# Kernel optimization log

Measured on AMD Instinct MI355X. Metric: run time of the kernel, lower is better.

The kernel has to match this reference:

```python
import jax, jax.numpy as jnp
import numpy as np

DIM = 1024
HEADS = 16
HEAD_DIM = DIM // HEADS
RANK = 16
ALPHA = 8.0
SCALING = ALPHA / RANK  # 0.5
SCALE = HEAD_DIM ** (-0.5)
B_, L_ = 2, 2048


def _proj_params(key, std=0.02):
    kW, kb, kA, kB = jax.random.split(key, 4)
    W = jax.random.normal(kW, (DIM, DIM), jnp.float32) * std   # [out, in]
    b = jax.random.normal(kb, (DIM,), jnp.float32) * std
    A = jax.random.normal(kA, (DIM, RANK), jnp.float32) * std  # [out, r]
    Bm = jax.random.normal(kB, (RANK, DIM), jnp.float32) * std # [r, in]
    return W, b, A, Bm


def setup_inputs() -> dict:
    key = jax.random.key(0)
    ks = jax.random.split(key, 6)
    x = jax.random.normal(ks[0], (B_, L_, DIM), jnp.float32)
    attn_bias = jax.random.normal(ks[1], (1, HEADS, L_, L_), jnp.float32) * 0.1
    inp = {"x": x, "attn_bias": attn_bias}
    for name, k in zip("qkvo", ks[2:6]):
        W, b, A, Bm = _proj_params(k)
        inp[f"W{name}"] = W
        inp[f"b{name}"] = b
        inp[f"A{name}"] = A
        inp[f"B{name}"] = Bm
    return inp


def _lora_linear(x, W, b, A, Bm):
    # y = x W^T + b + scaling * ((x @ A) @ B)   (matches torch LoRALinear)
    return x @ W.T + b + SCALING * ((x @ A) @ Bm)


def _split(x):
    B, L, D = x.shape
    return jnp.swapaxes(x.reshape(B, L, HEADS, HEAD_DIM), 1, 2)  # [B,H,L,hd]


def reference(x, attn_bias, Wq, bq, Aq, Bq, Wk, bk, Ak, Bk, Wv, bv, Av, Bv, Wo, bo, Ao, Bo):
    B, L, D = x.shape
    q = _split(_lora_linear(x, Wq, bq, Aq, Bq))
    k = _split(_lora_linear(x, Wk, bk, Ak, Bk))
    v = _split(_lora_linear(x, Wv, bv, Av, Bv))
    scores = jnp.einsum('bhld,bhmd->bhlm', q, k) * SCALE + attn_bias
    attn = jax.nn.softmax(scores, axis=-1)  # dropout p=0 -> identity
    out = jnp.einsum('bhlm,bhmd->bhld', attn, v)
    out = jnp.swapaxes(out, 1, 2).reshape(B, L, D)  # merge heads
    return _lora_linear(out, Wo, bo, Ao, Bo)
```

## Files before the change

### kernel.cpp

```cpp
#include <hip/hip_runtime.h>
#include <cstdint>

typedef __bf16 bf16;
typedef __bf16 bf16x8 __attribute__((ext_vector_type(8)));
typedef __bf16 bf16x4 __attribute__((ext_vector_type(4)));
typedef float  f32x4  __attribute__((ext_vector_type(4)));
typedef float  f32x16 __attribute__((ext_vector_type(16)));
typedef int    i32x4  __attribute__((ext_vector_type(4)));

#define DIM   1024
#define LSEQ  2048
#define NH    16
#define HD    64
#define NTOK  4096

#define AS1C(p) ((const __attribute__((address_space(1))) void*)(unsigned long long)(uintptr_t)(p))
#define AS3P(p) ((__attribute__((address_space(3))) void*)(unsigned int)(uintptr_t)(p))
#define SB0 __builtin_amdgcn_sched_barrier(0)

__device__ __forceinline__ f32x4 mfma16(bf16x8 a, bf16x8 b, f32x4 c) {
  return __builtin_amdgcn_mfma_f32_16x16x32_bf16(a, b, c, 0, 0, 0);
}
__device__ __forceinline__ f32x16 mfma32(bf16x8 a, bf16x8 b, f32x16 c) {
  return __builtin_amdgcn_mfma_f32_32x32x16_bf16(a, b, c, 0, 0, 0);
}
__device__ __forceinline__ int pk2(float a, float b) {
  unsigned short ua = __builtin_bit_cast(unsigned short, (bf16)a);
  unsigned short ub = __builtin_bit_cast(unsigned short, (bf16)b);
  return (int)ua | ((int)ub << 16);
}

__global__ __launch_bounds__(256) void k_cvt(const float* __restrict__ x,
                                             bf16* __restrict__ xb) {
  const int i = (blockIdx.x * 256 + threadIdx.x) * 4;
  const f32x4 v = *(const f32x4*)(x + i);
  bf16x4 o;
  o[0] = (bf16)v[0]; o[1] = (bf16)v[1]; o[2] = (bf16)v[2]; o[3] = (bf16)v[3];
  *(bf16x4*)(xb + i) = o;
}

struct WeffArgs {
  const float* W[4]; const float* A[4]; const float* B[4]; bf16* out[4];
};

__global__ __launch_bounds__(256) void k_weff(WeffArgs args) {
  const int o = blockIdx.x;
  const int z = blockIdx.y;
  const float* __restrict__ W  = args.W[z];
  const float* __restrict__ A  = args.A[z];
  const float* __restrict__ Bm = args.B[z];
  bf16* __restrict__ out = args.out[z];
  float Bo[16];
#pragma unroll
  for (int r = 0; r < 16; ++r) Bo[r] = Bm[r * DIM + o];
#pragma unroll
  for (int j = 0; j < 4; ++j) {
    const int d = j * 256 + (int)threadIdx.x;
    const float* Ar = A + (size_t)d * 16;
    float acc = 0.f;
#pragma unroll
    for (int r = 0; r < 16; ++r) acc += Ar[r] * Bo[r];
    out[(size_t)o * DIM + d] = (bf16)(W[(size_t)o * DIM + d] + 0.5f * acc);
  }
}

template <int NF, bool F32OUT>
__device__ __forceinline__ void gemm_body(const bf16* __restrict__ X,
                                          const bf16* __restrict__ W,
                                          const float* __restrict__ bias,
                                          void* __restrict__ out,
                                          float scale, int m0, int n0) {
  constexpr int BN = NF * 32;
  __shared__ __align__(16) bf16 As[128 * 32];
  __shared__ __align__(16) bf16 Bs[BN * 32];
  const int tid  = threadIdx.x;
  const int lane = tid & 63, w = tid >> 6;
  const int l15 = lane & 15, l4 = lane >> 4;
  const int wr = w >> 1, wc = w & 1;
  const int srow = w * 16 + (lane >> 2);
  const int scol = (lane & 3) * 8;

  f32x4 acc[4][NF] = {};
  const bf16* ag = X + (size_t)m0 * DIM;
  const bf16* bg = W + (size_t)n0 * DIM;

  for (int kt = 0; kt < DIM / 32; ++kt) {
    const int k0 = kt * 32;
#pragma unroll
    for (int j = 0; j < 2; ++j) {
      const int row = j * 64 + srow;
      __builtin_amdgcn_global_load_lds(AS1C(ag + (size_t)row * DIM + k0 + scol),
                                       AS3P(As + (j * 64 + w * 16) * 32), 16, 0, 0);
      if (j * 64 < BN)
        __builtin_amdgcn_global_load_lds(AS1C(bg + (size_t)row * DIM + k0 + scol),
                                         AS3P(Bs + (j * 64 + w * 16) * 32), 16, 0, 0);
    }
    __syncthreads();
    bf16x8 af[4], bfr[NF];
#pragma unroll
    for (int m = 0; m < 4; ++m)
      af[m] = *(const bf16x8*)(As + (wr * 64 + m * 16 + l15) * 32 + l4 * 8);
#pragma unroll
    for (int n = 0; n < NF; ++n)
      bfr[n] = *(const bf16x8*)(Bs + (wc * NF * 16 + n * 16 + l15) * 32 + l4 * 8);
#pragma unroll
    for (int m = 0; m < 4; ++m)
#pragma unroll
      for (int n = 0; n < NF; ++n)
        acc[m][n] = mfma16(af[m], bfr[n], acc[m][n]);
    __syncthreads();
  }

#pragma unroll
  for (int m = 0; m < 4; ++m) {
    const int r0 = m0 + wr * 64 + m * 16 + l4 * 4;
#pragma unroll
    for (int n = 0; n < NF; ++n) {
      const int c = n0 + wc * NF * 16 + n * 16 + l15;
      const float bc = bias[c];
#pragma unroll
      for (int t = 0; t < 4; ++t) {
        const float y = (acc[m][n][t] + bc) * scale;
        if constexpr (F32OUT)
          ((float*)out)[(size_t)(r0 + t) * DIM + c] = y;
        else
          ((bf16*)out)[(size_t)(r0 + t) * DIM + c] = (bf16)y;
      }
    }
  }
}

__global__ __launch_bounds__(256) void k_gemm_qkv(
    const bf16* __restrict__ xb, const bf16* __restrict__ weff,
    const float* __restrict__ bq, const float* __restrict__ bk,
    const float* __restrict__ bv,
    bf16* __restrict__ q, bf16* __restrict__ k, bf16* __restrict__ v) {
  const int z = blockIdx.z;
  const bf16* W = weff + (size_t)z * DIM * DIM;
  const float* bias = (z == 0) ? bq : (z == 1) ? bk : bv;
  bf16* out = (z == 0) ? q : (z == 1) ? k : v;
  const float scale = (z == 0) ? 0.125f : 1.0f;
  gemm_body<4, false>(xb, W, bias, out, scale, blockIdx.x * 128, blockIdx.y * 128);
}

__global__ __launch_bounds__(256) void k_gemm_o(
    const bf16* __restrict__ ctx, const bf16* __restrict__ weffo,
    const float* __restrict__ bo, float* __restrict__ out) {
  gemm_body<2, true>(ctx, weffo, bo, out, 1.0f, blockIdx.x * 128, blockIdx.y * 64);
}

__global__ __launch_bounds__(256) void k_vfrag(const bf16* __restrict__ v,
                                               const bf16* __restrict__ k,
                                               bf16* __restrict__ vf,
                                               bf16* __restrict__ kf) {
  const int lt = blockIdx.x, bh = blockIdx.y;
  const int b = bh >> 4, h = bh & 15;
  __shared__ __align__(16) bf16 tile[64][72];
  const int tid = threadIdx.x;
  const int r = tid >> 2, c0 = (tid & 3) * 16;
  const bf16* src = v + (size_t)(b * LSEQ + lt * 64) * DIM + h * HD;
  *(bf16x8*)(&tile[r][c0])     = *(const bf16x8*)(src + (size_t)r * DIM + c0);
  *(bf16x8*)(&tile[r][c0 + 8]) = *(const bf16x8*)(src + (size_t)r * DIM + c0 + 8);
  __syncthreads();
  const int w = tid >> 6, lane = tid & 63, l31 = lane & 31, hi = lane >> 5;
  {
    const int tt = w >> 1, n = w & 1;
    const int t = lt * 2 + tt;
#pragma unroll
    for (int c = 0; c < 2; ++c) {
      bf16 tmp[8];
#pragma unroll
      for (int j = 0; j < 8; ++j)
        tmp[j] = tile[tt * 32 + c * 16 + hi * 8 + j][n * 32 + l31];
      *(bf16x8*)(vf + ((((size_t)bh * 64 + t) * 4 + n * 2 + c) * 64 + lane) * 8) =
          *(bf16x8*)tmp;
    }
  }
  {
    const int t = lt * 2 + (w & 1);
    const bf16* krow = k + (size_t)(b * LSEQ + t * 32 + l31) * DIM + h * HD + hi * 8;
#pragma unroll
    for (int cc = 0; cc < 2; ++cc) {
      const int c = (w >> 1) + cc * 2;
      *(bf16x8*)(kf + ((((size_t)bh * 64 + t) * 4 + c) * 64 + lane) * 8) =
          *(const bf16x8*)(krow + c * 16);
    }
  }
}

__global__ __launch_bounds__(512, 1) void k_attn(
    const bf16* __restrict__ q, const bf16* __restrict__ kf,
    const bf16* __restrict__ vf, const float* __restrict__ bias,
    bf16* __restrict__ ctx) {
  const int tid = threadIdx.x, w = tid >> 6, lane = tid & 63;
  const int l31 = lane & 31, hi = lane >> 5;
  const int bb = w >> 2, qs = w & 3;
  const int h = blockIdx.x & 15;
  const int q0 = (blockIdx.x >> 4) * 128;

  __shared__ __align__(16) bf16  kls[2][4][2048];
  __shared__ __align__(16) bf16  vls[2][4][2048];
  __shared__ __align__(16) float bls[4][4096];

  const bf16* qrow = q + (size_t)(bb * LSEQ + q0 + qs * 32 + l31) * DIM + h * HD;
  bf16x8 Qf[4];
#pragma unroll
  for (int c = 0; c < 4; ++c) Qf[c] = *(const bf16x8*)(qrow + c * 16 + hi * 8);

  const int kvA = 2 * w, kvB = 2 * w + 1;
  const int kbA = kvA >> 3, vvA = (kvA >> 2) & 1, cA = kvA & 3;
  const int kbB = kvB >> 3, vvB = (kvB >> 2) & 1, cB = kvB & 3;
  const bf16* srcA = (vvA ? vf : kf) + (size_t)(kbA * NH + h) * 64 * 2048 + cA * 512 + lane * 8;
  const bf16* srcB = (vvB ? vf : kf) + (size_t)(kbB * NH + h) * 64 * 2048 + cB * 512 + lane * 8;
  bf16* dstA = (vvA ? &vls[kbA][0][0] : &kls[kbA][0][0]) + cA * 512 + lane * 8;
  bf16* dstB = (vvB ? &vls[kbB][0][0] : &kls[kbB][0][0]) + cB * 512 + lane * 8;
  const int lr = lane >> 3, lc = lane & 7;
  const float* bsA = bias + ((size_t)h * LSEQ + q0 + 16 * w + lr) * LSEQ + 4 * (lc ^ lr);
  const float* bsB = bsA + (size_t)8 * LSEQ;
  float* bdA = &bls[0][0] + (2 * w) * 256 + lane * 4;
  float* bdB = bdA + 256;

  f32x16 acc0 = {}, acc1 = {};
  float mrun = -3e38f, lrun = 0.f;

#define STAGE(t_, s_)                                                          \
  {                                                                            \
    __builtin_amdgcn_global_load_lds(AS1C(srcA + (size_t)(t_) * 2048),         \
                                     AS3P(dstA + (s_) * 2048), 16, 0, 0);      \
    __builtin_amdgcn_global_load_lds(AS1C(srcB + (size_t)(t_) * 2048),         \
                                     AS3P(dstB + (s_) * 2048), 16, 0, 0);      \
    __builtin_amdgcn_global_load_lds(AS1C(bsA + (size_t)(t_) * 32),            \
                                     AS3P(bdA + (s_) * 4096), 16, 0, 0);       \
    __builtin_amdgcn_global_load_lds(AS1C(bsB + (size_t)(t_) * 32),            \
                                     AS3P(bdB + (s_) * 4096), 16, 0, 0);       \
  }

  STAGE(0, 0); SB0;
  STAGE(1, 1); SB0;
  STAGE(2, 2); SB0;

  const int rr = qs * 32 + l31;
  const int sw = (l31 & 7) << 2;
  for (int t = 0; t < 64; ++t) {
    const int sl = t & 3;
    const int tn = (t + 3 > 63) ? 63 : t + 3;
    STAGE(tn, (t + 3) & 3); SB0;
    asm volatile("s_waitcnt vmcnt(12)" ::: "memory");
    __builtin_amdgcn_s_barrier();

    bf16x8 Kf[4], Vf[2][2];
    f32x4 br[4];
#pragma unroll
    for (int c = 0; c < 4; ++c)
      Kf[c] = *(const bf16x8*)(&kls[bb][sl][c * 512 + lane * 8]);
#pragma unroll
    for (int u = 0; u < 4; ++u)
      Vf[u >> 1][u & 1] = *(const bf16x8*)(&vls[bb][sl][u * 512 + lane * 8]);
#pragma unroll
    for (int g = 0; g < 4; ++g)
      br[g] = *(const f32x4*)(
          &bls[sl][rr * 32 + (((g << 3) | (hi << 2)) ^ sw)]);
    asm volatile("s_waitcnt lgkmcnt(0)" ::: "memory");
    SB0;
    __builtin_amdgcn_s_barrier();

    f32x16 s = {};
#pragma unroll
    for (int c = 0; c < 4; ++c) s = mfma32(Kf[c], Qf[c], s);
    float p[16];
#pragma unroll
    for (int r = 0; r < 16; ++r) p[r] = s[r] + br[r >> 2][r & 3];
    float m8[8];
#pragma unroll
    for (int i = 0; i < 8; ++i) m8[i] = fmaxf(p[i], p[i + 8]);
    float tm = fmaxf(fmaxf(fmaxf(m8[0], m8[4]), fmaxf(m8[1], m8[5])),
                     fmaxf(fmaxf(m8[2], m8[6]), fmaxf(m8[3], m8[7])));
    tm = fmaxf(tm, __shfl_xor(tm, 32));
    if (!__all(tm <= mrun + 8.0f)) {
      const float mn = fmaxf(mrun, tm);
      const float scl = __expf(mrun - mn);
      mrun = mn;
      lrun *= scl;
#pragma unroll
      for (int r = 0; r < 16; ++r) { acc0[r] *= scl; acc1[r] *= scl; }
    }
#pragma unroll
    for (int r = 0; r < 16; ++r) p[r] = __expf(p[r] - mrun);
    float s8[8];
#pragma unroll
    for (int i = 0; i < 8; ++i) s8[i] = p[i] + p[i + 8];
    float rs = ((s8[0] + s8[1]) + (s8[2] + s8[3])) + ((s8[4] + s8[5]) + (s8[6] + s8[7]));
    rs += __shfl_xor(rs, 32);
    lrun += rs;
#pragma unroll
    for (int c = 0; c < 2; ++c) {
      const int c8 = c * 8;
      const int A0 = pk2(p[c8 + 0], p[c8 + 1]);
      const int A1 = pk2(p[c8 + 2], p[c8 + 3]);
      const int B0 = pk2(p[c8 + 4], p[c8 + 5]);
      const int B1 = pk2(p[c8 + 6], p[c8 + 7]);
      const int pA0 = __shfl_xor(A0, 32), pA1 = __shfl_xor(A1, 32);
      const int pB0 = __shfl_xor(B0, 32), pB1 = __shfl_xor(B1, 32);
      i32x4 fi;
      fi[0] = hi ? pB0 : A0;
      fi[1] = hi ? pB1 : A1;
      fi[2] = hi ? B0 : pA0;
      fi[3] = hi ? B1 : pA1;
      const bf16x8 pf = __builtin_bit_cast(bf16x8, fi);
      acc0 = mfma32(Vf[0][c], pf, acc0);
      acc1 = mfma32(Vf[1][c], pf, acc1);
    }
  }
#undef STAGE

  const float inv = 1.0f / lrun;
  bf16* cp = ctx + (size_t)(bb * LSEQ + q0 + qs * 32 + l31) * DIM + h * HD;
#pragma unroll
  for (int r = 0; r < 16; ++r) {
    const int dr = (r & 3) + 8 * (r >> 2) + 4 * hi;
    cp[dr]      = (bf16)(acc0[r] * inv);
    cp[32 + dr] = (bf16)(acc1[r] * inv);
  }
}

extern "C" void kernel_launch(void* const* d_in, const int* in_sizes, int n_in,
                              void* d_out, int out_size, void* d_ws, size_t ws_size,
                              hipStream_t stream) {
  const float* x  = (const float*)d_in[0];
  const float* ab = (const float*)d_in[1];
  const float* Wq = (const float*)d_in[2];  const float* bq = (const float*)d_in[3];
  const float* Aq = (const float*)d_in[4];  const float* Bq = (const float*)d_in[5];
  const float* Wk = (const float*)d_in[6];  const float* bk = (const float*)d_in[7];
  const float* Ak = (const float*)d_in[8];  const float* Bk = (const float*)d_in[9];
  const float* Wv = (const float*)d_in[10]; const float* bv = (const float*)d_in[11];
  const float* Av = (const float*)d_in[12]; const float* Bv = (const float*)d_in[13];
  const float* Wo = (const float*)d_in[14]; const float* bo = (const float*)d_in[15];
  const float* Ao = (const float*)d_in[16]; const float* Bo = (const float*)d_in[17];

  uint8_t* ws = (uint8_t*)d_ws;
  const size_t SZ = (size_t)NTOK * DIM * sizeof(bf16);
  bf16* xb   = (bf16*)(ws + 0 * SZ);
  bf16* weff = (bf16*)(ws + 1 * SZ);
  bf16* qb   = (bf16*)(ws + 2 * SZ);
  bf16* kb   = (bf16*)(ws + 3 * SZ);
  bf16* vb   = (bf16*)(ws + 4 * SZ);
  bf16* kfb  = (bf16*)(ws + 5 * SZ);
  bf16* vfb  = (bf16*)(ws + 6 * SZ);
  bf16* ctx  = (bf16*)(ws + 7 * SZ);

  k_cvt<<<dim3(NTOK * DIM / 1024), 256, 0, stream>>>(x, xb);

  WeffArgs wa;
  wa.W[0] = Wq; wa.A[0] = Aq; wa.B[0] = Bq; wa.out[0] = weff;
  wa.W[1] = Wk; wa.A[1] = Ak; wa.B[1] = Bk; wa.out[1] = weff + (size_t)DIM * DIM;
  wa.W[2] = Wv; wa.A[2] = Av; wa.B[2] = Bv; wa.out[2] = weff + 2 * (size_t)DIM * DIM;
  wa.W[3] = Wo; wa.A[3] = Ao; wa.B[3] = Bo; wa.out[3] = weff + 3 * (size_t)DIM * DIM;
  k_weff<<<dim3(DIM, 4), 256, 0, stream>>>(wa);

  k_gemm_qkv<<<dim3(32, 8, 3), 256, 0, stream>>>(xb, weff, bq, bk, bv, qb, kb, vb);
  k_vfrag<<<dim3(32, 32), 256, 0, stream>>>(vb, kb, vfb, kfb);
  k_attn<<<dim3(256), 512, 0, stream>>>(qb, kfb, vfb, ab, ctx);
  k_gemm_o<<<dim3(32, 16), 256, 0, stream>>>(ctx, weff + 3 * (size_t)DIM * DIM, bo,
                                             (float*)d_out);
}
```

Baseline: 173.9 us.

## Double GEMM K-tile to 64 with XOR-swizzled LDS layout

The shared GEMM body now stages 64-wide K tiles instead of 32, which halves the number of barrier pairs per output tile and issues two MFMAs per fragment between barriers. LDS rows are XOR-swizzled by row index to avoid bank conflicts on the wider rows. The QKV grid is flattened from a 3D to a 2D launch over the concatenated weight matrix. LDS use per block doubles, which may lower occupancy.

```diff
diff --git a/kernel.cpp b/kernel.cpp
--- a/kernel.cpp
+++ b/kernel.cpp
@@ -65,49 +65,64 @@
 }
 
 template <int NF, bool F32OUT>
-__device__ __forceinline__ void gemm_body(const bf16* __restrict__ X,
-                                          const bf16* __restrict__ W,
-                                          const float* __restrict__ bias,
-                                          void* __restrict__ out,
-                                          float scale, int m0, int n0) {
+__device__ __forceinline__ void gemm_body64(const bf16* __restrict__ X,
+                                            const bf16* __restrict__ W,
+                                            const float* __restrict__ bias,
+                                            void* __restrict__ out,
+                                            float scale, int m0, int n0, int ncol0) {
   constexpr int BN = NF * 32;
-  __shared__ __align__(16) bf16 As[128 * 32];
-  __shared__ __align__(16) bf16 Bs[BN * 32];
+  constexpr int BJ = BN / 32;
+  __shared__ __align__(16) bf16 As[128 * 64];
+  __shared__ __align__(16) bf16 Bs[BN * 64];
   const int tid  = threadIdx.x;
   const int lane = tid & 63, w = tid >> 6;
   const int l15 = lane & 15, l4 = lane >> 4;
   const int wr = w >> 1, wc = w & 1;
-  const int srow = w * 16 + (lane >> 2);
-  const int scol = (lane & 3) * 8;
+  const int lr = lane >> 3;
+  const int scol = ((lane & 7) ^ lr) * 8;
 
   f32x4 acc[4][NF] = {};
   const bf16* ag = X + (size_t)m0 * DIM;
   const bf16* bg = W + (size_t)n0 * DIM;
 
-  for (int kt = 0; kt < DIM / 32; ++kt) {
-    const int k0 = kt * 32;
-#pragma unroll
-    for (int j = 0; j < 2; ++j) {
-      const int row = j * 64 + srow;
-      __builtin_amdgcn_global_load_lds(AS1C(ag + (size_t)row * DIM + k0 + scol),
-                                       AS3P(As + (j * 64 + w * 16) * 32), 16, 0, 0);
-      if (j * 64 < BN)
-        __builtin_amdgcn_global_load_lds(AS1C(bg + (size_t)row * DIM + k0 + scol),
-                                         AS3P(Bs + (j * 64 + w * 16) * 32), 16, 0, 0);
+  for (int kt = 0; kt < DIM / 64; ++kt) {
+    const int k0 = kt * 64;
+#pragma unroll
+    for (int j = 0; j < 4; ++j) {
+      const int rb = w * 4 + j;
+      __builtin_amdgcn_global_load_lds(
+          AS1C(ag + (size_t)(rb * 8 + lr) * DIM + k0 + scol),
+          AS3P(As + rb * 512), 16, 0, 0);
+    }
+#pragma unroll
+    for (int j = 0; j < BJ; ++j) {
+      const int rb = w * BJ + j;
+      __builtin_amdgcn_global_load_lds(
+          AS1C(bg + (size_t)(rb * 8 + lr) * DIM + k0 + scol),
+          AS3P(Bs + rb * 512), 16, 0, 0);
     }
     __syncthreads();
-    bf16x8 af[4], bfr[NF];
+    bf16x8 af[2][4], bfr[2][NF];
+#pragma unroll
+    for (int ks = 0; ks < 2; ++ks) {
+#pragma unroll
+      for (int m = 0; m < 4; ++m) {
+        const int r = wr * 64 + m * 16 + l15;
+        af[ks][m] = *(const bf16x8*)(As + r * 64 + ((ks * 4 + l4) ^ (r & 7)) * 8);
+      }
+#pragma unroll
+      for (int n = 0; n < NF; ++n) {
+        const int r = wc * (NF * 16) + n * 16 + l15;
+        bfr[ks][n] = *(const bf16x8*)(Bs + r * 64 + ((ks * 4 + l4) ^ (r & 7)) * 8);
+      }
+    }
 #pragma unroll
     for (int m = 0; m < 4; ++m)
-      af[m] = *(const bf16x8*)(As + (wr * 64 + m * 16 + l15) * 32 + l4 * 8);
-#pragma unroll
-    for (int n = 0; n < NF; ++n)
-      bfr[n] = *(const bf16x8*)(Bs + (wc * NF * 16 + n * 16 + l15) * 32 + l4 * 8);
-#pragma unroll
-    for (int m = 0; m < 4; ++m)
-#pragma unroll
-      for (int n = 0; n < NF; ++n)
-        acc[m][n] = mfma16(af[m], bfr[n], acc[m][n]);
+#pragma unroll
+      for (int n = 0; n < NF; ++n) {
+        acc[m][n] = mfma16(af[0][m], bfr[0][n], acc[m][n]);
+        acc[m][n] = mfma16(af[1][m], bfr[1][n], acc[m][n]);
+      }
     __syncthreads();
   }
 
@@ -116,7 +131,7 @@
     const int r0 = m0 + wr * 64 + m * 16 + l4 * 4;
 #pragma unroll
     for (int n = 0; n < NF; ++n) {
-      const int c = n0 + wc * NF * 16 + n * 16 + l15;
+      const int c = ncol0 + wc * (NF * 16) + n * 16 + l15;
       const float bc = bias[c];
 #pragma unroll
       for (int t = 0; t < 4; ++t) {
@@ -135,18 +150,19 @@
     const float* __restrict__ bq, const float* __restrict__ bk,
     const float* __restrict__ bv,
     bf16* __restrict__ q, bf16* __restrict__ k, bf16* __restrict__ v) {
-  const int z = blockIdx.z;
-  const bf16* W = weff + (size_t)z * DIM * DIM;
+  const int n0 = blockIdx.y * 128;
+  const int z = n0 >> 10;
   const float* bias = (z == 0) ? bq : (z == 1) ? bk : bv;
   bf16* out = (z == 0) ? q : (z == 1) ? k : v;
   const float scale = (z == 0) ? 0.125f : 1.0f;
-  gemm_body<4, false>(xb, W, bias, out, scale, blockIdx.x * 128, blockIdx.y * 128);
+  gemm_body64<4, false>(xb, weff, bias, out, scale, blockIdx.x * 128, n0, n0 & 1023);
 }
 
 __global__ __launch_bounds__(256) void k_gemm_o(
     const bf16* __restrict__ ctx, const bf16* __restrict__ weffo,
     const float* __restrict__ bo, float* __restrict__ out) {
-  gemm_body<2, true>(ctx, weffo, bo, out, 1.0f, blockIdx.x * 128, blockIdx.y * 64);
+  const int n0 = blockIdx.y * 64;
+  gemm_body64<2, true>(ctx, weffo, bo, out, 1.0f, blockIdx.x * 128, n0, n0);
 }
 
 __global__ __launch_bounds__(256) void k_vfrag(const bf16* __restrict__ v,
@@ -357,7 +373,7 @@
   wa.W[3] = Wo; wa.A[3] = Ao; wa.B[3] = Bo; wa.out[3] = weff + 3 * (size_t)DIM * DIM;
   k_weff<<<dim3(DIM, 4), 256, 0, stream>>>(wa);
 
-  k_gemm_qkv<<<dim3(32, 8, 3), 256, 0, stream>>>(xb, weff, bq, bk, bv, qb, kb, vb);
+  k_gemm_qkv<<<dim3(32, 24), 256, 0, stream>>>(xb, weff, bq, bk, bv, qb, kb, vb);
   k_vfrag<<<dim3(32, 32), 256, 0, stream>>>(vb, kb, vfb, kfb);
   k_attn<<<dim3(256), 512, 0, stream>>>(qb, kfb, vfb, ab, ctx);
   k_gemm_o<<<dim3(32, 16), 256, 0, stream>>>(ctx, weff + 3 * (size_t)DIM * DIM, bo,
```

Measured after the change: 170.3 us. -2.1%, faster.
